# Kernel optimization log

Measured on AMD Instinct MI355X. Metric: run time of the kernel, lower is better.

The kernel has to match this reference:

```python
import jax, jax.numpy as jnp
import numpy as np

N = 8192
IN_F = 256
OUT_F = 256
ALPHA = 0.2  # LeakyReLU negative slope
NEG_INF = -1e12


def setup_inputs() -> dict:
    key = jax.random.key(0)
    k1, k2, k3, k4, k5 = jax.random.split(key, 5)
    inp = jax.random.normal(k1, (N, IN_F), dtype=jnp.float32)
    adj = jax.random.randint(k2, (N, N), 0, 2, dtype=jnp.int32)
    # xavier_uniform with gain=1.414
    def xavier(k, shape, gain=1.414):
        fan_in, fan_out = shape[0], shape[1]
        bound = gain * np.sqrt(6.0 / (fan_in + fan_out))
        return jax.random.uniform(k, shape, jnp.float32, -bound, bound)
    W = xavier(k3, (IN_F, OUT_F))
    a = xavier(k4, (2 * OUT_F, 1))
    wtrans = xavier(k5, (2 * IN_F, OUT_F))
    return {"inp": inp, "adj": adj, "W": W, "a": a, "wtrans": wtrans}


def reference(inp, adj, W, a, wtrans):
    h = inp @ W                                  # [N, OUT_F]
    Wh1 = h @ a[:OUT_F, :]                       # [N, 1]
    Wh2 = h @ a[OUT_F:, :]                       # [N, 1]
    e = jax.nn.leaky_relu(Wh1 + Wh2.T, ALPHA)    # [N, N]
    mask = adj > 0
    attention = jax.nn.softmax(jnp.where(mask, e, NEG_INF), axis=1)
    negative_attention = -jax.nn.softmax(jnp.where(mask, -e, NEG_INF), axis=1)
    # dropout=0.0 / eval mode -> identity
    h_prime = attention @ inp                    # [N, IN_F]
    h_prime_negative = negative_attention @ inp  # [N, IN_F]
    h_prime_double = jnp.concatenate([h_prime, h_prime_negative], axis=1)
    new_h_prime = h_prime_double @ wtrans        # [N, OUT_F]
    return jax.nn.elu(new_h_prime)               # concat=True
```

## Files before the change

kernel.cpp:

```cpp
#include <hip/hip_runtime.h>
#include <stdint.h>

#define GN 8192
#define LOG2E 1.4426950408889634f

typedef float f32x4 __attribute__((ext_vector_type(4)));
typedef short s16x8 __attribute__((ext_vector_type(8)));
typedef unsigned short u16x8 __attribute__((ext_vector_type(8)));
typedef int i32x4 __attribute__((ext_vector_type(4)));

__device__ __forceinline__ unsigned short f2bf(float f) {
    unsigned int u = __float_as_uint(f);
    u += 0x7FFFu + ((u >> 16) & 1u);
    return (unsigned short)(u >> 16);
}
__device__ __forceinline__ float bf2f(unsigned short h) {
    return __uint_as_float(((unsigned int)h) << 16);
}

__global__ void kA(const float* __restrict__ W, const float* __restrict__ a,
                   float* __restrict__ w1, float* __restrict__ w2) {
    int k = blockIdx.x, l = threadIdx.x;
    float s1 = 0.f, s2 = 0.f;
#pragma unroll
    for (int q = 0; q < 4; ++q) {
        int o = l + q * 64;
        float w = W[k * 256 + o];
        s1 += w * a[o];
        s2 += w * a[256 + o];
    }
#pragma unroll
    for (int off = 32; off; off >>= 1) {
        s1 += __shfl_xor(s1, off);
        s2 += __shfl_xor(s2, off);
    }
    if (l == 0) {
        w1[k] = s1 * LOG2E;
        w2[k] = s2 * LOG2E;
    }
}

__global__ __launch_bounds__(256) void kA2(const float* __restrict__ wt,
                                           unsigned short* __restrict__ wtT) {
    __shared__ unsigned short Tt[32][33];
    const int bi = blockIdx.x;
    const int bj = blockIdx.y;
    const int ty = threadIdx.x >> 3, tx8 = threadIdx.x & 7;
    float4 v = *(const float4*)(wt + (size_t)(bj * 32 + ty) * 256 + bi * 32 + tx8 * 4);
    Tt[tx8 * 4 + 0][ty] = f2bf(v.x);
    Tt[tx8 * 4 + 1][ty] = f2bf(v.y);
    Tt[tx8 * 4 + 2][ty] = f2bf(v.z);
    Tt[tx8 * 4 + 3][ty] = f2bf(v.w);
    __syncthreads();
    ushort4 o4;
    o4.x = Tt[ty][tx8 * 4 + 0];
    o4.y = Tt[ty][tx8 * 4 + 1];
    o4.z = Tt[ty][tx8 * 4 + 2];
    o4.w = Tt[ty][tx8 * 4 + 3];
    *(ushort4*)(wtT + (size_t)(bi * 32 + ty) * 512 + bj * 32 + tx8 * 4) = o4;
}

__global__ __launch_bounds__(256) void kB(const float* __restrict__ inp,
                                          const float* __restrict__ w1,
                                          const float* __restrict__ w2,
                                          float* __restrict__ s, float* __restrict__ t,
                                          unsigned short* __restrict__ inpT) {
    __shared__ unsigned short T[256][33];
    const int tid = threadIdx.x;
    const int r0 = blockIdx.x * 32;
    const int r = tid >> 3, cs = tid & 7;
    const float4* in4 = (const float4*)(inp + (size_t)(r0 + r) * 256 + cs * 32);
    const float4* w14 = (const float4*)(w1 + cs * 32);
    const float4* w24 = (const float4*)(w2 + cs * 32);
    float zs = 0.f, zt = 0.f;
#pragma unroll
    for (int q = 0; q < 8; ++q) {
        float4 v = in4[q];
        float4 a1 = w14[q];
        float4 a2 = w24[q];
        zs += v.x * a1.x + v.y * a1.y + v.z * a1.z + v.w * a1.w;
        zt += v.x * a2.x + v.y * a2.y + v.z * a2.z + v.w * a2.w;
        int c = cs * 32 + q * 4;
        T[c + 0][r] = f2bf(v.x);
        T[c + 1][r] = f2bf(v.y);
        T[c + 2][r] = f2bf(v.z);
        T[c + 3][r] = f2bf(v.w);
    }
#pragma unroll
    for (int off = 1; off < 8; off <<= 1) {
        zs += __shfl_xor(zs, off);
        zt += __shfl_xor(zt, off);
    }
    if (cs == 0) {
        s[r0 + r] = zs;
        t[r0 + r] = zt;
    }
    __syncthreads();
    unsigned short* dst = inpT + (size_t)tid * GN + r0;
    ushort4* d4 = (ushort4*)dst;
#pragma unroll
    for (int q = 0; q < 8; ++q) {
        ushort4 v;
        v.x = T[tid][q * 4 + 0];
        v.y = T[tid][q * 4 + 1];
        v.z = T[tid][q * 4 + 2];
        v.w = T[tid][q * 4 + 3];
        d4[q] = v;
    }
}

#define PROCB(Q, TX, BP, BN)                          \
    {                                                 \
        float e = sr + (TX);                          \
        float l = fmaxf(e, 0.2f * e);                 \
        bool on = (m8 & (1u << (Q))) != 0u;           \
        float p1 = on ? exp2f(l) : 0.f;               \
        float p2 = on ? exp2f(-l) : 0.f;              \
        unsigned short b1 = f2bf(p1);                 \
        unsigned short b2 = f2bf(p2);                 \
        zp += bf2f(b1);                               \
        zn += bf2f(b2);                               \
        BP = b1;                                      \
        BN = b2;                                      \
    }

__global__ __launch_bounds__(512, 2) void kC(const int* __restrict__ adj,
                                             const float* __restrict__ sv,
                                             const float* __restrict__ tv,
                                             const unsigned short* __restrict__ inpT,
                                             const unsigned short* __restrict__ wtT,
                                             float* __restrict__ out) {
    __shared__ __align__(16) char smem[33792];
    __shared__ float Zpart[256];
    __shared__ float Zs[32];
    const int tid = threadIdx.x;
    const int lane = tid & 63, w = tid >> 6;
    const int rr = lane & 15, hi = lane >> 4;
    const int lr = tid >> 5, lc8 = tid & 31;
    const int i0 = blockIdx.x * 16;
    const float sr = sv[i0 + rr];
    float zp = 0.f, zn = 0.f;
    f32x4 accP[2], accN[2];
    accP[0] = (f32x4)(0.f);
    accP[1] = (f32x4)(0.f);
    accN[0] = (f32x4)(0.f);
    accN[1] = (f32x4)(0.f);
    const int fb = w * 32;
    const size_t rowb0 = (size_t)(fb + rr) * GN;
    const size_t rowb1 = (size_t)(fb + 16 + rr) * GN;
    const size_t arowb = (size_t)(i0 + lr) * GN + lc8 * 8;
    const int tspan = w * 32 + hi * 8;
    const int pwoff = w * 1024 + lane * 16;
    const int proff = lane * 16;
    const int moff = 32768;
    const int mrd = rr * 32 + w * 4 + hi;

    {
        i32x4 a0 = *(const i32x4*)(adj + arowb);
        i32x4 a1 = *(const i32x4*)(adj + arowb + 4);
        unsigned nm = (a0.x ? 1u : 0u) | (a0.y ? 2u : 0u) | (a0.z ? 4u : 0u) | (a0.w ? 8u : 0u) |
                      (a1.x ? 16u : 0u) | (a1.y ? 32u : 0u) | (a1.z ? 64u : 0u) | (a1.w ? 128u : 0u);
        *(unsigned char*)(smem + moff + tid) = (unsigned char)nm;
    }
    float4 tf0 = *(const float4*)(tv + tspan);
    float4 tf1 = *(const float4*)(tv + tspan + 4);
    __syncthreads();

    for (int jc = 0; jc < 32; ++jc) {
        const int b8 = (jc & 1) * 8192;
        const size_t jcoff = (size_t)jc * 256;
        float4 tc0 = tf0, tc1 = tf1;
        i32x4 ca0, ca1;
        if (jc < 31) {
            const int* an = adj + arowb + (jc + 1) * 256;
            ca0 = *(const i32x4*)an;
            ca1 = *(const i32x4*)(an + 4);
            const float* tn = tv + (jc + 1) * 256 + tspan;
            tf0 = *(const float4*)tn;
            tf1 = *(const float4*)(tn + 4);
        }
        s16x8 bA[8];
#pragma unroll
        for (int kc = 0; kc < 4; ++kc) {
            bA[kc * 2 + 0] = *(const s16x8*)(inpT + rowb0 + jcoff + kc * 32 + hi * 8);
            bA[kc * 2 + 1] = *(const s16x8*)(inpT + rowb1 + jcoff + kc * 32 + hi * 8);
        }
        __builtin_amdgcn_sched_barrier(0);
        unsigned m8 = (unsigned)*(volatile unsigned char*)(smem + moff + (jc & 1) * 512 + mrd);
        u16x8 up, un;
        PROCB(0, tc0.x, up[0], un[0]);
        PROCB(1, tc0.y, up[1], un[1]);
        PROCB(2, tc0.z, up[2], un[2]);
        PROCB(3, tc0.w, up[3], un[3]);
        PROCB(4, tc1.x, up[4], un[4]);
        PROCB(5, tc1.y, up[5], un[5]);
        PROCB(6, tc1.z, up[6], un[6]);
        PROCB(7, tc1.w, up[7], un[7]);
        *(u16x8*)(smem + b8 + pwoff) = up;
        *(u16x8*)(smem + 16384 + b8 + pwoff) = un;
        if (jc < 31) {
            unsigned nm = (ca0.x ? 1u : 0u) | (ca0.y ? 2u : 0u) | (ca0.z ? 4u : 0u) | (ca0.w ? 8u : 0u) |
                          (ca1.x ? 16u : 0u) | (ca1.y ? 32u : 0u) | (ca1.z ? 64u : 0u) | (ca1.w ? 128u : 0u);
            *(unsigned char*)(smem + moff + ((jc + 1) & 1) * 512 + tid) = (unsigned char)nm;
        }
        asm volatile("s_waitcnt lgkmcnt(0)" ::: "memory");
        __builtin_amdgcn_s_barrier();
        asm volatile("" ::: "memory");
        s16x8 bB[8];
#pragma unroll
        for (int kc = 4; kc < 8; ++kc) {
            bB[(kc - 4) * 2 + 0] = *(const s16x8*)(inpT + rowb0 + jcoff + kc * 32 + hi * 8);
            bB[(kc - 4) * 2 + 1] = *(const s16x8*)(inpT + rowb1 + jcoff + kc * 32 + hi * 8);
        }
        __builtin_amdgcn_sched_barrier(0);
#pragma unroll
        for (int kc = 0; kc < 4; ++kc) {
            s16x8 aP = *(const s16x8*)(smem + b8 + kc * 1024 + proff);
            s16x8 aN = *(const s16x8*)(smem + 16384 + b8 + kc * 1024 + proff);
            accP[0] = __builtin_amdgcn_mfma_f32_16x16x32_bf16(aP, bA[kc * 2 + 0], accP[0], 0, 0, 0);
            accP[1] = __builtin_amdgcn_mfma_f32_16x16x32_bf16(aP, bA[kc * 2 + 1], accP[1], 0, 0, 0);
            accN[0] = __builtin_amdgcn_mfma_f32_16x16x32_bf16(aN, bA[kc * 2 + 0], accN[0], 0, 0, 0);
            accN[1] = __builtin_amdgcn_mfma_f32_16x16x32_bf16(aN, bA[kc * 2 + 1], accN[1], 0, 0, 0);
        }
#pragma unroll
        for (int kc = 4; kc < 8; ++kc) {
            s16x8 aP = *(const s16x8*)(smem + b8 + kc * 1024 + proff);
            s16x8 aN = *(const s16x8*)(smem + 16384 + b8 + kc * 1024 + proff);
            accP[0] = __builtin_amdgcn_mfma_f32_16x16x32_bf16(aP, bB[(kc - 4) * 2 + 0], accP[0], 0, 0, 0);
            accP[1] = __builtin_amdgcn_mfma_f32_16x16x32_bf16(aP, bB[(kc - 4) * 2 + 1], accP[1], 0, 0, 0);
            accN[0] = __builtin_amdgcn_mfma_f32_16x16x32_bf16(aN, bB[(kc - 4) * 2 + 0], accN[0], 0, 0, 0);
            accN[1] = __builtin_amdgcn_mfma_f32_16x16x32_bf16(aN, bB[(kc - 4) * 2 + 1], accN[1], 0, 0, 0);
        }
    }
    zp += __shfl_xor(zp, 16);
    zp += __shfl_xor(zp, 32);
    zn += __shfl_xor(zn, 16);
    zn += __shfl_xor(zn, 32);
    if (lane < 16) {
        Zpart[w * 16 + rr] = zp;
        Zpart[128 + w * 16 + rr] = zn;
    }
    __syncthreads();
    if (tid < 32) {
        int which = tid >> 4, row = tid & 15;
        float z = 0.f;
#pragma unroll
        for (int w2 = 0; w2 < 8; ++w2) z += Zpart[which * 128 + w2 * 16 + row];
        Zs[which * 16 + row] = z;
    }
    __syncthreads();
    char* hdl = smem;
#pragma unroll
    for (int reg = 0; reg < 4; ++reg) {
        int row = hi * 4 + reg;
        float izp = 1.f / Zs[row];
        float izn = 1.f / Zs[16 + row];
        int sw = (row & 7) << 4;
#pragma unroll
        for (int nt = 0; nt < 2; ++nt) {
            int col = fb + nt * 16 + rr;
            *(unsigned short*)(hdl + ((row * 1024 + col * 2) ^ sw)) =
                f2bf(accP[nt][reg] * izp);
            *(unsigned short*)(hdl + ((row * 1024 + (col + 256) * 2) ^ sw)) =
                f2bf(-accN[nt][reg] * izn);
        }
    }
    __syncthreads();
    f32x4 oc[2];
    oc[0] = (f32x4)(0.f);
    oc[1] = (f32x4)(0.f);
#pragma unroll
    for (int kc = 0; kc < 16; ++kc) {
        int rb = (rr * 1024 + kc * 64 + hi * 16) ^ ((rr & 7) << 4);
        s16x8 av = *(const s16x8*)(hdl + rb);
#pragma unroll
        for (int nt = 0; nt < 2; ++nt) {
            s16x8 b = *(const s16x8*)(wtT + (size_t)(fb + nt * 16 + rr) * 512 + kc * 32 + hi * 8);
            oc[nt] = __builtin_amdgcn_mfma_f32_16x16x32_bf16(av, b, oc[nt], 0, 0, 0);
        }
    }
#pragma unroll
    for (int nt = 0; nt < 2; ++nt) {
        int col = fb + nt * 16 + rr;
#pragma unroll
        for (int reg = 0; reg < 4; ++reg) {
            int row = i0 + hi * 4 + reg;
            float x = oc[nt][reg];
            out[(size_t)row * 256 + col] = x > 0.f ? x : __expf(x) - 1.f;
        }
    }
}

extern "C" void kernel_launch(void* const* d_in, const int* in_sizes, int n_in,
                              void* d_out, int out_size, void* d_ws, size_t ws_size,
                              hipStream_t stream) {
    const float* inp = (const float*)d_in[0];
    const int* adj = (const int*)d_in[1];
    const float* W = (const float*)d_in[2];
    const float* a = (const float*)d_in[3];
    const float* wt = (const float*)d_in[4];
    float* out = (float*)d_out;
    char* ws = (char*)d_ws;

    unsigned short* inpT = (unsigned short*)ws;
    float* s = (float*)(ws + (4 << 20));
    float* t = (float*)(ws + (4 << 20) + (1 << 15));
    float* w1 = (float*)(ws + (4 << 20) + (2 << 15));
    float* w2 = (float*)(ws + (4 << 20) + (2 << 15) + 4096);
    unsigned short* wtT = (unsigned short*)(ws + (4 << 20) + (2 << 15) + 8192);

    hipLaunchKernelGGL(kA, dim3(256), dim3(64), 0, stream, W, a, w1, w2);
    hipLaunchKernelGGL(kA2, dim3(8, 16), dim3(256), 0, stream, wt, wtT);
    hipLaunchKernelGGL(kB, dim3(256), dim3(256), 0, stream, inp, w1, w2, s, t, inpT);
    hipLaunchKernelGGL(kC, dim3(512), dim3(512), 0, stream, adj, s, t, inpT, wtT, out);
}
```

Before: 562.0 us.

## Process 32 query rows per block to reuse inpT fragments across two M tiles

Each block of kC now covers 32 attention rows instead of 16, so every inpT B-fragment loaded from global memory feeds twice as many MFMAs. This halves the total inpT traffic, which was re-read by every row block. The adjacency mask prefetch is widened to 16 ints per thread and moved two chunks ahead. The cost is doubled LDS usage, more registers, and half the grid (256 blocks on the device), with launch bounds relaxed so occupancy may drop.

```diff
diff --git a/kernel.cpp b/kernel.cpp
--- a/kernel.cpp
+++ b/kernel.cpp
@@ -109,186 +109,241 @@
     }
 }
 
-#define PROCB(Q, TX, BP, BN)                          \
+#define PROCQ(Q, SR, TX, M8, ZP, ZN, BP, BN)          \
     {                                                 \
-        float e = sr + (TX);                          \
+        float e = (SR) + (TX);                        \
         float l = fmaxf(e, 0.2f * e);                 \
-        bool on = (m8 & (1u << (Q))) != 0u;           \
+        bool on = ((M8) & (1u << (Q))) != 0u;         \
         float p1 = on ? exp2f(l) : 0.f;               \
         float p2 = on ? exp2f(-l) : 0.f;              \
         unsigned short b1 = f2bf(p1);                 \
         unsigned short b2 = f2bf(p2);                 \
-        zp += bf2f(b1);                               \
-        zn += bf2f(b2);                               \
+        ZP += bf2f(b1);                               \
+        ZN += bf2f(b2);                               \
         BP = b1;                                      \
         BN = b2;                                      \
     }
 
-__global__ __launch_bounds__(512, 2) void kC(const int* __restrict__ adj,
-                                             const float* __restrict__ sv,
-                                             const float* __restrict__ tv,
-                                             const unsigned short* __restrict__ inpT,
-                                             const unsigned short* __restrict__ wtT,
-                                             float* __restrict__ out) {
-    __shared__ __align__(16) char smem[33792];
-    __shared__ float Zpart[256];
-    __shared__ float Zs[32];
+#define PACK16(A0, A1, A2, A3)                                                          \
+    ((unsigned)((A0.x ? 1u : 0u) | (A0.y ? 2u : 0u) | (A0.z ? 4u : 0u) | (A0.w ? 8u : 0u) | \
+                (A1.x ? 16u : 0u) | (A1.y ? 32u : 0u) | (A1.z ? 64u : 0u) | (A1.w ? 128u : 0u) | \
+                (A2.x ? 256u : 0u) | (A2.y ? 512u : 0u) | (A2.z ? 1024u : 0u) | (A2.w ? 2048u : 0u) | \
+                (A3.x ? 4096u : 0u) | (A3.y ? 8192u : 0u) | (A3.z ? 16384u : 0u) | (A3.w ? 32768u : 0u)))
+
+__global__ __launch_bounds__(512) void kC(const int* __restrict__ adj,
+                                          const float* __restrict__ sv,
+                                          const float* __restrict__ tv,
+                                          const unsigned short* __restrict__ inpT,
+                                          const unsigned short* __restrict__ wtT,
+                                          float* __restrict__ out) {
+    __shared__ __align__(16) char smem[67840];
+    __shared__ float Zpart[512];
+    __shared__ float Zs[64];
     const int tid = threadIdx.x;
     const int lane = tid & 63, w = tid >> 6;
-    const int rr = lane & 15, hi = lane >> 4;
-    const int lr = tid >> 5, lc8 = tid & 31;
-    const int i0 = blockIdx.x * 16;
-    const float sr = sv[i0 + rr];
-    float zp = 0.f, zn = 0.f;
-    f32x4 accP[2], accN[2];
-    accP[0] = (f32x4)(0.f);
-    accP[1] = (f32x4)(0.f);
-    accN[0] = (f32x4)(0.f);
-    accN[1] = (f32x4)(0.f);
+    const int rr = lane & 15, hi = (lane >> 4) & 3;
+    const int lr = tid >> 4, lc = tid & 15;
+    const int i0 = blockIdx.x * 32;
+    const float sr0 = sv[i0 + rr];
+    const float sr1 = sv[i0 + 16 + rr];
+    float zp0 = 0.f, zp1 = 0.f, zn0 = 0.f, zn1 = 0.f;
+    f32x4 accP[2][2], accN[2][2];
+#pragma unroll
+    for (int m = 0; m < 2; ++m)
+#pragma unroll
+        for (int n = 0; n < 2; ++n) {
+            accP[m][n] = (f32x4)(0.f);
+            accN[m][n] = (f32x4)(0.f);
+        }
     const int fb = w * 32;
     const size_t rowb0 = (size_t)(fb + rr) * GN;
     const size_t rowb1 = (size_t)(fb + 16 + rr) * GN;
-    const size_t arowb = (size_t)(i0 + lr) * GN + lc8 * 8;
+    const size_t arowb = (size_t)(i0 + lr) * GN + lc * 16;
     const int tspan = w * 32 + hi * 8;
-    const int pwoff = w * 1024 + lane * 16;
-    const int proff = lane * 16;
-    const int moff = 32768;
-    const int mrd = rr * 32 + w * 4 + hi;
+    const int NOFF = 32768, MOFF = 65536;
+    const int pw = w * 1024 + lane * 16;
+    const int pr = lane * 16;
+    const int mwr = lr * 36 + lc * 2;
+    const int mrd0 = rr * 36 + w * 4 + hi;
+    const int mrd1 = (16 + rr) * 36 + w * 4 + hi;
 
     {
-        i32x4 a0 = *(const i32x4*)(adj + arowb);
-        i32x4 a1 = *(const i32x4*)(adj + arowb + 4);
-        unsigned nm = (a0.x ? 1u : 0u) | (a0.y ? 2u : 0u) | (a0.z ? 4u : 0u) | (a0.w ? 8u : 0u) |
-                      (a1.x ? 16u : 0u) | (a1.y ? 32u : 0u) | (a1.z ? 64u : 0u) | (a1.w ? 128u : 0u);
-        *(unsigned char*)(smem + moff + tid) = (unsigned char)nm;
+        const int* ap = adj + arowb;
+        i32x4 a0 = *(const i32x4*)ap;
+        i32x4 a1 = *(const i32x4*)(ap + 4);
+        i32x4 a2 = *(const i32x4*)(ap + 8);
+        i32x4 a3 = *(const i32x4*)(ap + 12);
+        *(unsigned short*)(smem + MOFF + mwr) = (unsigned short)PACK16(a0, a1, a2, a3);
+    }
+    i32x4 caF0, caF1, caF2, caF3;
+    {
+        const int* ap = adj + arowb + 256;
+        caF0 = *(const i32x4*)ap;
+        caF1 = *(const i32x4*)(ap + 4);
+        caF2 = *(const i32x4*)(ap + 8);
+        caF3 = *(const i32x4*)(ap + 12);
     }
     float4 tf0 = *(const float4*)(tv + tspan);
     float4 tf1 = *(const float4*)(tv + tspan + 4);
     __syncthreads();
 
     for (int jc = 0; jc < 32; ++jc) {
-        const int b8 = (jc & 1) * 8192;
+        const int b16 = (jc & 1) * 16384;
         const size_t jcoff = (size_t)jc * 256;
         float4 tc0 = tf0, tc1 = tf1;
-        i32x4 ca0, ca1;
+        s16x8 bA[8], bB[8];
+#pragma unroll
+        for (int kc = 0; kc < 4; ++kc) {
+            bA[kc * 2 + 0] = *(const s16x8*)(inpT + rowb0 + jcoff + kc * 32 + hi * 8);
+            bA[kc * 2 + 1] = *(const s16x8*)(inpT + rowb1 + jcoff + kc * 32 + hi * 8);
+        }
+#pragma unroll
+        for (int kc = 4; kc < 8; ++kc) {
+            bB[(kc - 4) * 2 + 0] = *(const s16x8*)(inpT + rowb0 + jcoff + kc * 32 + hi * 8);
+            bB[(kc - 4) * 2 + 1] = *(const s16x8*)(inpT + rowb1 + jcoff + kc * 32 + hi * 8);
+        }
         if (jc < 31) {
-            const int* an = adj + arowb + (jc + 1) * 256;
-            ca0 = *(const i32x4*)an;
-            ca1 = *(const i32x4*)(an + 4);
+            *(unsigned short*)(smem + MOFF + ((jc + 1) & 1) * 1152 + mwr) =
+                (unsigned short)PACK16(caF0, caF1, caF2, caF3);
+        }
+        if (jc < 30) {
+            const int* ap = adj + arowb + (jc + 2) * 256;
+            caF0 = *(const i32x4*)ap;
+            caF1 = *(const i32x4*)(ap + 4);
+            caF2 = *(const i32x4*)(ap + 8);
+            caF3 = *(const i32x4*)(ap + 12);
+        }
+        if (jc < 31) {
             const float* tn = tv + (jc + 1) * 256 + tspan;
             tf0 = *(const float4*)tn;
             tf1 = *(const float4*)(tn + 4);
         }
-        s16x8 bA[8];
-#pragma unroll
-        for (int kc = 0; kc < 4; ++kc) {
-            bA[kc * 2 + 0] = *(const s16x8*)(inpT + rowb0 + jcoff + kc * 32 + hi * 8);
-            bA[kc * 2 + 1] = *(const s16x8*)(inpT + rowb1 + jcoff + kc * 32 + hi * 8);
-        }
-        __builtin_amdgcn_sched_barrier(0);
-        unsigned m8 = (unsigned)*(volatile unsigned char*)(smem + moff + (jc & 1) * 512 + mrd);
-        u16x8 up, un;
-        PROCB(0, tc0.x, up[0], un[0]);
-        PROCB(1, tc0.y, up[1], un[1]);
-        PROCB(2, tc0.z, up[2], un[2]);
-        PROCB(3, tc0.w, up[3], un[3]);
-        PROCB(4, tc1.x, up[4], un[4]);
-        PROCB(5, tc1.y, up[5], un[5]);
-        PROCB(6, tc1.z, up[6], un[6]);
-        PROCB(7, tc1.w, up[7], un[7]);
-        *(u16x8*)(smem + b8 + pwoff) = up;
-        *(u16x8*)(smem + 16384 + b8 + pwoff) = un;
-        if (jc < 31) {
-            unsigned nm = (ca0.x ? 1u : 0u) | (ca0.y ? 2u : 0u) | (ca0.z ? 4u : 0u) | (ca0.w ? 8u : 0u) |
-                          (ca1.x ? 16u : 0u) | (ca1.y ? 32u : 0u) | (ca1.z ? 64u : 0u) | (ca1.w ? 128u : 0u);
-            *(unsigned char*)(smem + moff + ((jc + 1) & 1) * 512 + tid) = (unsigned char)nm;
-        }
+        unsigned m8a = (unsigned)*(volatile unsigned char*)(smem + MOFF + (jc & 1) * 1152 + mrd0);
+        unsigned m8b = (unsigned)*(volatile unsigned char*)(smem + MOFF + (jc & 1) * 1152 + mrd1);
+        u16x8 up0, up1, un0, un1;
+        PROCQ(0, sr0, tc0.x, m8a, zp0, zn0, up0[0], un0[0]);
+        PROCQ(1, sr0, tc0.y, m8a, zp0, zn0, up0[1], un0[1]);
+        PROCQ(2, sr0, tc0.z, m8a, zp0, zn0, up0[2], un0[2]);
+        PROCQ(3, sr0, tc0.w, m8a, zp0, zn0, up0[3], un0[3]);
+        PROCQ(4, sr0, tc1.x, m8a, zp0, zn0, up0[4], un0[4]);
+        PROCQ(5, sr0, tc1.y, m8a, zp0, zn0, up0[5], un0[5]);
+        PROCQ(6, sr0, tc1.z, m8a, zp0, zn0, up0[6], un0[6]);
+        PROCQ(7, sr0, tc1.w, m8a, zp0, zn0, up0[7], un0[7]);
+        PROCQ(0, sr1, tc0.x, m8b, zp1, zn1, up1[0], un1[0]);
+        PROCQ(1, sr1, tc0.y, m8b, zp1, zn1, up1[1], un1[1]);
+        PROCQ(2, sr1, tc0.z, m8b, zp1, zn1, up1[2], un1[2]);
+        PROCQ(3, sr1, tc0.w, m8b, zp1, zn1, up1[3], un1[3]);
+        PROCQ(4, sr1, tc1.x, m8b, zp1, zn1, up1[4], un1[4]);
+        PROCQ(5, sr1, tc1.y, m8b, zp1, zn1, up1[5], un1[5]);
+        PROCQ(6, sr1, tc1.z, m8b, zp1, zn1, up1[6], un1[6]);
+        PROCQ(7, sr1, tc1.w, m8b, zp1, zn1, up1[7], un1[7]);
+        *(u16x8*)(smem + b16 + pw) = up0;
+        *(u16x8*)(smem + b16 + 8192 + pw) = up1;
+        *(u16x8*)(smem + NOFF + b16 + pw) = un0;
+        *(u16x8*)(smem + NOFF + b16 + 8192 + pw) = un1;
         asm volatile("s_waitcnt lgkmcnt(0)" ::: "memory");
         __builtin_amdgcn_s_barrier();
         asm volatile("" ::: "memory");
-        s16x8 bB[8];
+#pragma unroll
+        for (int kc = 0; kc < 4; ++kc) {
+            s16x8 aP0 = *(const s16x8*)(smem + b16 + kc * 1024 + pr);
+            s16x8 aP1 = *(const s16x8*)(smem + b16 + 8192 + kc * 1024 + pr);
+            s16x8 aN0 = *(const s16x8*)(smem + NOFF + b16 + kc * 1024 + pr);
+            s16x8 aN1 = *(const s16x8*)(smem + NOFF + b16 + 8192 + kc * 1024 + pr);
+            s16x8 b0 = bA[kc * 2 + 0], b1 = bA[kc * 2 + 1];
+            accP[0][0] = __builtin_amdgcn_mfma_f32_16x16x32_bf16(aP0, b0, accP[0][0], 0, 0, 0);
+            accP[0][1] = __builtin_amdgcn_mfma_f32_16x16x32_bf16(aP0, b1, accP[0][1], 0, 0, 0);
+            accP[1][0] = __builtin_amdgcn_mfma_f32_16x16x32_bf16(aP1, b0, accP[1][0], 0, 0, 0);
+            accP[1][1] = __builtin_amdgcn_mfma_f32_16x16x32_bf16(aP1, b1, accP[1][1], 0, 0, 0);
+            accN[0][0] = __builtin_amdgcn_mfma_f32_16x16x32_bf16(aN0, b0, accN[0][0], 0, 0, 0);
+            accN[0][1] = __builtin_amdgcn_mfma_f32_16x16x32_bf16(aN0, b1, accN[0][1], 0, 0, 0);
+            accN[1][0] = __builtin_amdgcn_mfma_f32_16x16x32_bf16(aN1, b0, accN[1][0], 0, 0, 0);
+            accN[1][1] = __builtin_amdgcn_mfma_f32_16x16x32_bf16(aN1, b1, accN[1][1], 0, 0, 0);
+        }
 #pragma unroll
         for (int kc = 4; kc < 8; ++kc) {
-            bB[(kc - 4) * 2 + 0] = *(const s16x8*)(inpT + rowb0 + jcoff + kc * 32 + hi * 8);
-            bB[(kc - 4) * 2 + 1] = *(const s16x8*)(inpT + rowb1 + jcoff + kc * 32 + hi * 8);
-        }
-        __builtin_amdgcn_sched_barrier(0);
-#pragma unroll
-        for (int kc = 0; kc < 4; ++kc) {
-            s16x8 aP = *(const s16x8*)(smem + b8 + kc * 1024 + proff);
-            s16x8 aN = *(const s16x8*)(smem + 16384 + b8 + kc * 1024 + proff);
-            accP[0] = __builtin_amdgcn_mfma_f32_16x16x32_bf16(aP, bA[kc * 2 + 0], accP[0], 0, 0, 0);
-            accP[1] = __builtin_amdgcn_mfma_f32_16x16x32_bf16(aP, bA[kc * 2 + 1], accP[1], 0, 0, 0);
-            accN[0] = __builtin_amdgcn_mfma_f32_16x16x32_bf16(aN, bA[kc * 2 + 0], accN[0], 0, 0, 0);
-            accN[1] = __builtin_amdgcn_mfma_f32_16x16x32_bf16(aN, bA[kc * 2 + 1], accN[1], 0, 0, 0);
-        }
-#pragma unroll
-        for (int kc = 4; kc < 8; ++kc) {
-            s16x8 aP = *(const s16x8*)(smem + b8 + kc * 1024 + proff);
-            s16x8 aN = *(const s16x8*)(smem + 16384 + b8 + kc * 1024 + proff);
-            accP[0] = __builtin_amdgcn_mfma_f32_16x16x32_bf16(aP, bB[(kc - 4) * 2 + 0], accP[0], 0, 0, 0);
-            accP[1] = __builtin_amdgcn_mfma_f32_16x16x32_bf16(aP, bB[(kc - 4) * 2 + 1], accP[1], 0, 0, 0);
-            accN[0] = __builtin_amdgcn_mfma_f32_16x16x32_bf16(aN, bB[(kc - 4) * 2 + 0], accN[0], 0, 0, 0);
-            accN[1] = __builtin_amdgcn_mfma_f32_16x16x32_bf16(aN, bB[(kc - 4) * 2 + 1], accN[1], 0, 0, 0);
-        }
-    }
-    zp += __shfl_xor(zp, 16);
-    zp += __shfl_xor(zp, 32);
-    zn += __shfl_xor(zn, 16);
-    zn += __shfl_xor(zn, 32);
+            s16x8 aP0 = *(const s16x8*)(smem + b16 + kc * 1024 + pr);
+            s16x8 aP1 = *(const s16x8*)(smem + b16 + 8192 + kc * 1024 + pr);
+            s16x8 aN0 = *(const s16x8*)(smem + NOFF + b16 + kc * 1024 + pr);
+            s16x8 aN1 = *(const s16x8*)(smem + NOFF + b16 + 8192 + kc * 1024 + pr);
+            s16x8 b0 = bB[(kc - 4) * 2 + 0], b1 = bB[(kc - 4) * 2 + 1];
+            accP[0][0] = __builtin_amdgcn_mfma_f32_16x16x32_bf16(aP0, b0, accP[0][0], 0, 0, 0);
+            accP[0][1] = __builtin_amdgcn_mfma_f32_16x16x32_bf16(aP0, b1, accP[0][1], 0, 0, 0);
+            accP[1][0] = __builtin_amdgcn_mfma_f32_16x16x32_bf16(aP1, b0, accP[1][0], 0, 0, 0);
+            accP[1][1] = __builtin_amdgcn_mfma_f32_16x16x32_bf16(aP1, b1, accP[1][1], 0, 0, 0);
+            accN[0][0] = __builtin_amdgcn_mfma_f32_16x16x32_bf16(aN0, b0, accN[0][0], 0, 0, 0);
+            accN[0][1] = __builtin_amdgcn_mfma_f32_16x16x32_bf16(aN0, b1, accN[0][1], 0, 0, 0);
+            accN[1][0] = __builtin_amdgcn_mfma_f32_16x16x32_bf16(aN1, b0, accN[1][0], 0, 0, 0);
+            accN[1][1] = __builtin_amdgcn_mfma_f32_16x16x32_bf16(aN1, b1, accN[1][1], 0, 0, 0);
+        }
+    }
+    zp0 += __shfl_xor(zp0, 16); zp0 += __shfl_xor(zp0, 32);
+    zp1 += __shfl_xor(zp1, 16); zp1 += __shfl_xor(zp1, 32);
+    zn0 += __shfl_xor(zn0, 16); zn0 += __shfl_xor(zn0, 32);
+    zn1 += __shfl_xor(zn1, 16); zn1 += __shfl_xor(zn1, 32);
     if (lane < 16) {
-        Zpart[w * 16 + rr] = zp;
-        Zpart[128 + w * 16 + rr] = zn;
-    }
-    __syncthreads();
-    if (tid < 32) {
-        int which = tid >> 4, row = tid & 15;
+        Zpart[0 * 128 + w * 16 + rr] = zp0;
+        Zpart[1 * 128 + w * 16 + rr] = zp1;
+        Zpart[2 * 128 + w * 16 + rr] = zn0;
+        Zpart[3 * 128 + w * 16 + rr] = zn1;
+    }
+    __syncthreads();
+    if (tid < 64) {
+        int cat = tid >> 4, row = tid & 15;
         float z = 0.f;
 #pragma unroll
-        for (int w2 = 0; w2 < 8; ++w2) z += Zpart[which * 128 + w2 * 16 + row];
-        Zs[which * 16 + row] = z;
+        for (int wv = 0; wv < 8; ++wv) z += Zpart[cat * 128 + wv * 16 + row];
+        Zs[(cat & 1) * 16 + (cat >> 1) * 32 + row] = z;
     }
     __syncthreads();
     char* hdl = smem;
 #pragma unroll
-    for (int reg = 0; reg < 4; ++reg) {
-        int row = hi * 4 + reg;
-        float izp = 1.f / Zs[row];
-        float izn = 1.f / Zs[16 + row];
-        int sw = (row & 7) << 4;
+    for (int m = 0; m < 2; ++m)
+#pragma unroll
+        for (int reg = 0; reg < 4; ++reg) {
+            int row = m * 16 + hi * 4 + reg;
+            float izp = 1.f / Zs[row];
+            float izn = 1.f / Zs[32 + row];
+            int sw = (row & 7) << 4;
+#pragma unroll
+            for (int nt = 0; nt < 2; ++nt) {
+                int col = fb + nt * 16 + rr;
+                *(unsigned short*)(hdl + ((row * 1024 + col * 2) ^ sw)) =
+                    f2bf(accP[m][nt][reg] * izp);
+                *(unsigned short*)(hdl + ((row * 1024 + (col + 256) * 2) ^ sw)) =
+                    f2bf(-accN[m][nt][reg] * izn);
+            }
+        }
+    __syncthreads();
+    f32x4 oc[2][2];
+#pragma unroll
+    for (int m = 0; m < 2; ++m)
+#pragma unroll
+        for (int nt = 0; nt < 2; ++nt) oc[m][nt] = (f32x4)(0.f);
+#pragma unroll
+    for (int kc = 0; kc < 16; ++kc) {
+        int rbs = (rr & 7) << 4;
+        s16x8 a0 = *(const s16x8*)(hdl + ((rr * 1024 + kc * 64 + hi * 16) ^ rbs));
+        s16x8 a1 = *(const s16x8*)(hdl + (((16 + rr) * 1024 + kc * 64 + hi * 16) ^ rbs));
+#pragma unroll
+        for (int nt = 0; nt < 2; ++nt) {
+            s16x8 b = *(const s16x8*)(wtT + (size_t)(fb + nt * 16 + rr) * 512 + kc * 32 + hi * 8);
+            oc[0][nt] = __builtin_amdgcn_mfma_f32_16x16x32_bf16(a0, b, oc[0][nt], 0, 0, 0);
+            oc[1][nt] = __builtin_amdgcn_mfma_f32_16x16x32_bf16(a1, b, oc[1][nt], 0, 0, 0);
+        }
+    }
+#pragma unroll
+    for (int m = 0; m < 2; ++m)
 #pragma unroll
         for (int nt = 0; nt < 2; ++nt) {
             int col = fb + nt * 16 + rr;
-            *(unsigned short*)(hdl + ((row * 1024 + col * 2) ^ sw)) =
-                f2bf(accP[nt][reg] * izp);
-            *(unsigned short*)(hdl + ((row * 1024 + (col + 256) * 2) ^ sw)) =
-                f2bf(-accN[nt][reg] * izn);
-        }
-    }
-    __syncthreads();
-    f32x4 oc[2];
-    oc[0] = (f32x4)(0.f);
-    oc[1] = (f32x4)(0.f);
-#pragma unroll
-    for (int kc = 0; kc < 16; ++kc) {
-        int rb = (rr * 1024 + kc * 64 + hi * 16) ^ ((rr & 7) << 4);
-        s16x8 av = *(const s16x8*)(hdl + rb);
-#pragma unroll
-        for (int nt = 0; nt < 2; ++nt) {
-            s16x8 b = *(const s16x8*)(wtT + (size_t)(fb + nt * 16 + rr) * 512 + kc * 32 + hi * 8);
-            oc[nt] = __builtin_amdgcn_mfma_f32_16x16x32_bf16(av, b, oc[nt], 0, 0, 0);
-        }
-    }
-#pragma unroll
-    for (int nt = 0; nt < 2; ++nt) {
-        int col = fb + nt * 16 + rr;
-#pragma unroll
-        for (int reg = 0; reg < 4; ++reg) {
-            int row = i0 + hi * 4 + reg;
-            float x = oc[nt][reg];
-            out[(size_t)row * 256 + col] = x > 0.f ? x : __expf(x) - 1.f;
-        }
-    }
+#pragma unroll
+            for (int reg = 0; reg < 4; ++reg) {
+                int row = i0 + m * 16 + hi * 4 + reg;
+                float x = oc[m][nt][reg];
+                out[(size_t)row * 256 + col] = x > 0.f ? x : __expf(x) - 1.f;
+            }
+        }
 }
 
 extern "C" void kernel_launch(void* const* d_in, const int* in_sizes, int n_in,
@@ -312,5 +367,5 @@
     hipLaunchKernelGGL(kA, dim3(256), dim3(64), 0, stream, W, a, w1, w2);
     hipLaunchKernelGGL(kA2, dim3(8, 16), dim3(256), 0, stream, wt, wtT);
     hipLaunchKernelGGL(kB, dim3(256), dim3(256), 0, stream, inp, w1, w2, s, t, inpT);
-    hipLaunchKernelGGL(kC, dim3(512), dim3(512), 0, stream, adj, s, t, inpT, wtT, out);
-}
+    hipLaunchKernelGGL(kC, dim3(256), dim3(512), 0, stream, adj, s, t, inpT, wtT, out);
+}
```

New measurement: 501.3 us. -10.8%, faster.
